# Kernel optimization log

Hardware: AMD Instinct MI355X
Metric: run time of the kernel (lower is better)

## Reference

```python
import jax, jax.numpy as jnp
import numpy as np
import math

PATCH = 16
IMG = 224
HEADS = 12
EMB = 768
HEAD_DIM = EMB // HEADS
SCALE = 1.0 / math.sqrt(HEAD_DIM)
NEG = -1.0e9


def _make_masks():
    n = IMG // PATCH  # patches per side
    centers = np.arange(n) * PATCH + PATCH / 2.0
    rows = np.repeat(centers, n)  # token center rows, length n*n
    cols = np.tile(centers, n)    # token center cols
    left = (cols[:, None] < cols[None, :]).astype(np.float32)
    right = (cols[:, None] > cols[None, :]).astype(np.float32)
    up = (rows[:, None] < rows[None, :]).astype(np.float32)
    down = (rows[:, None] > rows[None, :]).astype(np.float32)
    ident = np.eye(n * n, dtype=np.float32)
    pad = lambda m: np.pad(m, ((1, 0), (1, 0)))  # prepend CLS row/col of zeros
    return [jnp.asarray(pad(m)) for m in (left, right, up, down, ident)]

MASKS = _make_masks()  # 5 masks, each [N, N] with N = 197


def setup_inputs() -> dict:
    key = jax.random.key(0)
    ks = jax.random.split(key, 18)
    B, N = 32, (IMG // PATCH) ** 2 + 1
    w = lambda k: jax.random.normal(k, (EMB, EMB), jnp.float32) * 0.02
    b = lambda k: jax.random.normal(k, (EMB,), jnp.float32) * 0.02
    return {
        'x': jax.random.normal(ks[0], (B, N, EMB), jnp.float32),
        'q_w': w(ks[1]), 'q_b': b(ks[2]),
        'kA_w': w(ks[3]), 'kA_b': b(ks[4]),
        'kB_w': w(ks[5]), 'kB_b': b(ks[6]),
        'kC_w': w(ks[7]), 'kC_b': b(ks[8]),
        'kD_w': w(ks[9]), 'kD_b': b(ks[10]),
        'kE_w': w(ks[11]), 'kE_b': b(ks[12]),
        'v_w': w(ks[13]), 'v_b': b(ks[14]),
        'proj_w': w(ks[15]), 'proj_b': b(ks[16]),
    }


def reference(x, q_w, q_b, kA_w, kA_b, kB_w, kB_b, kC_w, kC_b, kD_w, kD_b,
              kE_w, kE_b, v_w, v_b, proj_w, proj_b):
    B, N, _ = x.shape
    # torch Linear: y = x @ W.T + b; then [B,N,H,D] -> [B,H,N,D]
    lin = lambda w, b_: (x @ w.T + b_).reshape(B, N, HEADS, HEAD_DIM).transpose(0, 2, 1, 3)
    q = lin(q_w, q_b) * SCALE
    v = lin(v_w, v_b)
    out = jnp.zeros_like(v)
    k_params = [(kA_w, kA_b), (kB_w, kB_b), (kC_w, kC_b), (kD_w, kD_b), (kE_w, kE_b)]
    for (kw, kb), mask in zip(k_params, MASKS):
        k = lin(kw, kb)
        scores = jnp.einsum('bhnd,bhmd->bhnm', q, k) + (1.0 - mask) * NEG
        out = out + jnp.einsum('bhnm,bhmd->bhnd', jax.nn.softmax(scores, axis=-1), v)
    out = out.transpose(0, 2, 1, 3).reshape(B, N, EMB)
    return out @ proj_w.T + proj_b
```

## Files before the change

### kernel.cpp

```cpp
#include <hip/hip_runtime.h>
#include <stdint.h>

typedef unsigned short u16;
typedef __bf16 bf16x8 __attribute__((ext_vector_type(8)));
typedef float f32x4 __attribute__((ext_vector_type(4)));

#define KDIM   768
#define MP     6400
#define MREAL  6304
#define SLOT   ((size_t)MP * KDIM)
#define WSZ    ((size_t)KDIM * KDIM)
#define QSCALE_L 0.18033688011112042f
#define BIGL     1.4426950e9f

struct Ptr9 { const float* p[9]; };
struct Ptr7 { const float* p[7]; };

__device__ __forceinline__ u16 f2b(float f) {
  uint32_t x = __float_as_uint(f);
  x += 0x7FFFu + ((x >> 16) & 1u);
  return (u16)(x >> 16);
}

__device__ __forceinline__ float b2f(u16 v) {
  return __uint_as_float(((uint32_t)v) << 16);
}

__device__ __forceinline__ void async16(const void* g, void* l) {
  __builtin_amdgcn_global_load_lds(
      (__attribute__((address_space(1))) void*)(uintptr_t)g,
      (__attribute__((address_space(3))) void*)l, 16, 0, 0);
}

__global__ __launch_bounds__(256) void k_convert(Ptr9 src, u16* __restrict__ xb,
                                                 u16* __restrict__ wall) {
  const int XN4 = MREAL * KDIM / 4;
  const int WN4 = (int)(WSZ / 4);
  const int total = XN4 + 8 * WN4;
  for (int i = blockIdx.x * blockDim.x + threadIdx.x; i < total;
       i += gridDim.x * blockDim.x) {
    const float4* sp; ushort4* dp; int off;
    if (i < XN4) { sp = (const float4*)src.p[0]; dp = (ushort4*)xb; off = i; }
    else {
      int t = i - XN4; int slot = t / WN4; off = t - slot * WN4;
      sp = (const float4*)src.p[1 + slot];
      dp = (ushort4*)(wall + (size_t)slot * WSZ);
    }
    float4 v = sp[off];
    ushort4 u;
    u.x = f2b(v.x); u.y = f2b(v.y); u.z = f2b(v.z); u.w = f2b(v.w);
    dp[off] = u;
  }
}

__global__ __launch_bounds__(256) void k_gemm(const u16* __restrict__ A,
                                              const u16* __restrict__ W,
                                              Ptr7 bias,
                                              u16* __restrict__ outb,
                                              float* __restrict__ outf,
                                              float scale0, int guard) {
  __shared__ u16 As[128 * 32];
  __shared__ u16 Bs[128 * 32];
  const int tid = threadIdx.x;
  const int w = tid >> 6, lane = tid & 63;
  const int li = lane & 15, g = lane >> 4;
  const int brow = blockIdx.x, bcol = blockIdx.y, z = blockIdx.z;
  const u16* Wz = W + (size_t)z * WSZ;
  const float* bz = bias.p[z];
  const int wr = (w >> 1) * 64, wc = (w & 1) * 64;
  f32x4 acc[4][4] = {};

  for (int k0 = 0; k0 < KDIM; k0 += 32) {
    __syncthreads();
#pragma unroll
    for (int c = 0; c < 2; ++c) {
      int cbase = (c * 4 + w) * 64;
      int chunk = cbase + lane;
      int row = chunk >> 2, kg = chunk & 3;
      async16(A  + (size_t)(brow * 128 + row) * KDIM + k0 + kg * 8,
              (char*)As + cbase * 16);
      async16(Wz + (size_t)(bcol * 128 + row) * KDIM + k0 + kg * 8,
              (char*)Bs + cbase * 16);
    }
    asm volatile("s_waitcnt vmcnt(0)" ::: "memory");
    __syncthreads();

    bf16x8 af[4], bfr[4];
#pragma unroll
    for (int i = 0; i < 4; ++i) {
      af[i]  = *(const bf16x8*)(As + (wr + i * 16 + li) * 32 + g * 8);
      bfr[i] = *(const bf16x8*)(Bs + (wc + i * 16 + li) * 32 + g * 8);
    }
#pragma unroll
    for (int i = 0; i < 4; ++i)
#pragma unroll
      for (int j = 0; j < 4; ++j)
        acc[i][j] = __builtin_amdgcn_mfma_f32_16x16x32_bf16(af[i], bfr[j],
                                                            acc[i][j], 0, 0, 0);
  }

  const float scz = (z == 0) ? scale0 : 1.0f;
  if (outf == nullptr) {
    u16* O = outb + (size_t)z * SLOT;
#pragma unroll
    for (int j = 0; j < 4; ++j) {
      int col = bcol * 128 + wc + j * 16 + li;
      float bsv = bz[col];
#pragma unroll
      for (int i = 0; i < 4; ++i) {
        int row = brow * 128 + wr + i * 16 + g * 4;
#pragma unroll
        for (int r = 0; r < 4; ++r)
          O[(size_t)(row + r) * KDIM + col] = f2b((acc[i][j][r] + bsv) * scz);
      }
    }
  } else {
#pragma unroll
    for (int j = 0; j < 4; ++j) {
      int col = bcol * 128 + wc + j * 16 + li;
      float bsv = bz[col];
#pragma unroll
      for (int i = 0; i < 4; ++i) {
        int row = brow * 128 + wr + i * 16 + g * 4;
#pragma unroll
        for (int r = 0; r < 4; ++r)
          if (row + r < guard)
            outf[(size_t)(row + r) * KDIM + col] = acc[i][j][r] + bsv;
      }
    }
  }
}

__global__ __launch_bounds__(512, 4) void k_attn(const u16* __restrict__ qkv,
                                                 u16* __restrict__ att) {
  __shared__ u16 KL[208 * 64];
  __shared__ u16 VT[64][228];
  __shared__ u16 P[2][8][16][36];
  const int tid = threadIdx.x;
  const int w = tid >> 6, lane = tid & 63;
  const int li = lane & 15, g = lane >> 4;
  const int bx = blockIdx.x, h = blockIdx.y, b = blockIdx.z;
  const int rt = bx * 8 + w;
  const size_t rowbase = (size_t)b * 197;
  const int cb = h * 64;
  const u16* Q = qkv;
  const u16* V = qkv + 6 * SLOT;
  const bool task = (rt <= 12);
  const int nmask = (bx == 0) ? 5 : 4;

  auto stageK = [&](int m) {
    const u16* Kg = qkv + (size_t)(1 + m) * SLOT;
#pragma unroll
    for (int i = 0; i < 4; ++i) {
      int cb64 = (i * 8 + w) * 64;
      if (cb64 >= 1664) break;
      int c = cb64 + lane;
      int row = c >> 3;
      int kg = (c & 7) ^ (row & 7);
      async16(Kg + (rowbase + row) * KDIM + cb + kg * 8,
              (char*)KL + cb64 * 16);
    }
  };

  stageK(0);

  for (int e = tid; e < 64 * 228; e += 512) {
    int j = e >> 6, d = e & 63;
    u16 val = 0;
    if (j < 197) val = V[(rowbase + j) * KDIM + cb + d];
    VT[d][j] = val;
  }

  const int i_ = rt * 16 + li;
  const int pi = i_ - 1;
  const int ri = pi / 14, ci = pi % 14;
  const bool i0 = (i_ == 0);

  const int rs_init = (g * 4 - 1) / 14;
  const int cs_init = (g * 4 - 1) % 14;

  bf16x8 qa0, qa1;
  {
    const size_t qrow = rowbase + (size_t)rt * 16 + li;
    qa0 = *(const bf16x8*)(Q + qrow * KDIM + cb + g * 8);
    qa1 = *(const bf16x8*)(Q + qrow * KDIM + cb + 32 + g * 8);
  }

  f32x4 oacc[4] = {};

  for (int m = 0; m < nmask; ++m) {
    asm volatile("s_waitcnt vmcnt(0)" ::: "memory");
    __syncthreads();

    const bool doit = task && (m < 4 || rt == 0);
    f32x4 s[13];
    if (doit) {
      __builtin_amdgcn_s_setprio(1);
#pragma unroll
      for (int t = 0; t < 13; ++t) {
        const char* base = (const char*)KL + (size_t)(t * 16 + li) * 128;
        const int sw = (li & 7) << 4;
        bf16x8 kb0 = *(const bf16x8*)(base + ((g * 16) ^ sw));
        bf16x8 kb1 = *(const bf16x8*)(base + ((64 + g * 16) ^ sw));
        f32x4 zz = {};
        zz = __builtin_amdgcn_mfma_f32_16x16x32_bf16(kb0, qa0, zz, 0, 0, 0);
        zz = __builtin_amdgcn_mfma_f32_16x16x32_bf16(kb1, qa1, zz, 0, 0, 0);
        s[t] = zz;
      }
      __builtin_amdgcn_s_setprio(0);
    }
    __syncthreads();
    if (m + 1 < nmask) stageK(m + 1);

    if (doit) {
      float mx = -3.0e38f;
      int cs = cs_init, rs = rs_init;
#pragma unroll
      for (int t = 0; t < 13; ++t) {
        int jv = t * 16 + g * 4;
        int cjr = cs, rjr = rs;
#pragma unroll
        for (int r = 0; r < 4; ++r) {
          bool mk;
          if (m == 0)      mk = ci < cjr;
          else if (m == 1) mk = ci > cjr;
          else if (m == 2) mk = ri < rjr;
          else if (m == 3) mk = ri > rjr;
          else             mk = (i_ == jv);
          if (i0 | (jv == 0)) mk = false;
          float sv = s[t][r] - (mk ? 0.f : BIGL);
          if (jv >= 197) sv = -3.0e38f;
          s[t][r] = sv;
          mx = fmaxf(mx, sv);
          ++jv; ++cjr; if (cjr == 14) { cjr = 0; ++rjr; }
        }
        cs += 2; ++rs; if (cs >= 14) { cs -= 14; ++rs; }
      }
      mx = fmaxf(mx, __shfl_xor(mx, 16));
      mx = fmaxf(mx, __shfl_xor(mx, 32));
      float sum = 0.f;
#pragma unroll
      for (int t = 0; t < 13; ++t)
#pragma unroll
        for (int r = 0; r < 4; ++r) {
          float e_ = exp2f(s[t][r] - mx);
          s[t][r] = e_;
          sum += e_;
        }
      sum += __shfl_xor(sum, 16);
      sum += __shfl_xor(sum, 32);
      const float inv = 1.0f / sum;

#pragma unroll
      for (int kt = 0; kt <= 7; ++kt) {
        if (kt < 7) {
#pragma unroll
          for (int h2 = 0; h2 < 2; ++h2) {
            const int t = kt * 2 + h2;
            uint32_t w0 = 0, w1 = 0;
            if (t < 13) {
              float a0 = s[t][0] * inv, a1 = s[t][1] * inv;
              float a2 = s[t][2] * inv, a3 = s[t][3] * inv;
              asm("v_cvt_pk_bf16_f32 %0, %1, %2" : "=v"(w0) : "v"(a0), "v"(a1));
              asm("v_cvt_pk_bf16_f32 %0, %1, %2" : "=v"(w1) : "v"(a2), "v"(a3));
            }
            uint2 pw; pw.x = w0; pw.y = w1;
            *(uint2*)&P[kt & 1][w][li][h2 * 16 + g * 4] = pw;
          }
        }
        if (kt > 0) {
          const int kr = kt - 1;
          bf16x8 pa = *(const bf16x8*)&P[kr & 1][w][li][g * 8];
          __builtin_amdgcn_s_setprio(1);
#pragma unroll
          for (int dt = 0; dt < 4; ++dt) {
            bf16x8 vb = *(const bf16x8*)&VT[dt * 16 + li][kr * 32 + g * 8];
            oacc[dt] = __builtin_amdgcn_mfma_f32_16x16x32_bf16(pa, vb, oacc[dt],
                                                               0, 0, 0);
          }
          __builtin_amdgcn_s_setprio(0);
        }
      }
    }
  }

  if (task && rt > 0) {
#pragma unroll
    for (int dt = 0; dt < 4; ++dt)
#pragma unroll
      for (int r = 0; r < 4; ++r) {
        int i2 = rt * 16 + g * 4 + r;
        oacc[dt][r] += b2f(VT[dt * 16 + li][i2]);
      }
  }

  if (task) {
#pragma unroll
    for (int dt = 0; dt < 4; ++dt)
#pragma unroll
      for (int r = 0; r < 4; ++r) {
        int i2 = rt * 16 + g * 4 + r;
        if (i2 < 197)
          att[(rowbase + i2) * KDIM + cb + dt * 16 + li] = f2b(oacc[dt][r]);
      }
  }
}

extern "C" void kernel_launch(void* const* d_in, const int* in_sizes, int n_in,
                              void* d_out, int out_size, void* d_ws, size_t ws_size,
                              hipStream_t stream) {
  (void)in_sizes; (void)n_in; (void)out_size; (void)ws_size;
  const float* x      = (const float*)d_in[0];
  const float* q_w    = (const float*)d_in[1];
  const float* q_b    = (const float*)d_in[2];
  const float* kA_w   = (const float*)d_in[3];
  const float* kA_b   = (const float*)d_in[4];
  const float* kB_w   = (const float*)d_in[5];
  const float* kB_b   = (const float*)d_in[6];
  const float* kC_w   = (const float*)d_in[7];
  const float* kC_b   = (const float*)d_in[8];
  const float* kD_w   = (const float*)d_in[9];
  const float* kD_b   = (const float*)d_in[10];
  const float* kE_w   = (const float*)d_in[11];
  const float* kE_b   = (const float*)d_in[12];
  const float* v_w    = (const float*)d_in[13];
  const float* v_b    = (const float*)d_in[14];
  const float* proj_w = (const float*)d_in[15];
  const float* proj_b = (const float*)d_in[16];
  float* out = (float*)d_out;

  u16* xb   = (u16*)d_ws;
  u16* qkv  = xb + SLOT;
  u16* wall = qkv + 7 * SLOT;
  u16* att  = xb;

  Ptr9 cs;
  cs.p[0] = x;    cs.p[1] = q_w;  cs.p[2] = kA_w; cs.p[3] = kB_w;
  cs.p[4] = kC_w; cs.p[5] = kD_w; cs.p[6] = kE_w; cs.p[7] = v_w;
  cs.p[8] = proj_w;
  k_convert<<<dim3(2048), dim3(256), 0, stream>>>(cs, xb, wall);

  Ptr7 b1;
  b1.p[0] = q_b;  b1.p[1] = kA_b; b1.p[2] = kB_b; b1.p[3] = kC_b;
  b1.p[4] = kD_b; b1.p[5] = kE_b; b1.p[6] = v_b;
  k_gemm<<<dim3(50, 6, 7), dim3(256), 0, stream>>>(xb, wall, b1, qkv, nullptr,
                                                   QSCALE_L, 0);

  k_attn<<<dim3(2, 12, 32), dim3(512), 0, stream>>>(qkv, att);

  Ptr7 b2;
  for (int i = 0; i < 7; ++i) b2.p[i] = proj_b;
  k_gemm<<<dim3(50, 6, 1), dim3(256), 0, stream>>>(att, wall + 7 * WSZ, b2,
                                                   nullptr, out, 1.0f, MREAL);
}
```

Baseline: 241.7 us.

## Keep softmax probabilities in registers by permuting V layout, drop P shared buffer

Removes the shared-memory round trip for the probability matrix. The softmax outputs are packed directly into MFMA A-operand registers, and V^T is stored in shared memory in a key-permuted, XOR-swizzled order that matches this register layout. It also vectorizes the V staging loads, shrinks the K and V shared buffers so the block needs less LDS, and raises the launch-bounds occupancy hint from 4 to 6. The permuted indexing adds address arithmetic and scattered 2-byte LDS stores during staging, and the higher occupancy target may constrain registers.

```diff
diff --git a/kernel.cpp b/kernel.cpp
--- a/kernel.cpp
+++ b/kernel.cpp
@@ -131,11 +131,11 @@
   }
 }
 
-__global__ __launch_bounds__(512, 4) void k_attn(const u16* __restrict__ qkv,
+__global__ __launch_bounds__(512, 6) void k_attn(const u16* __restrict__ qkv,
                                                  u16* __restrict__ att) {
-  __shared__ u16 KL[208 * 64];
-  __shared__ u16 VT[64][228];
-  __shared__ u16 P[2][8][16][36];
+  __shared__ u16 SM[200 * 64 + 64 * 224];
+  u16* KL = SM;
+  char* VTc = (char*)(SM + 200 * 64);
   const int tid = threadIdx.x;
   const int w = tid >> 6, lane = tid & 63;
   const int li = lane & 15, g = lane >> 4;
@@ -153,22 +153,34 @@
 #pragma unroll
     for (int i = 0; i < 4; ++i) {
       int cb64 = (i * 8 + w) * 64;
-      if (cb64 >= 1664) break;
-      int c = cb64 + lane;
-      int row = c >> 3;
-      int kg = (c & 7) ^ (row & 7);
-      async16(Kg + (rowbase + row) * KDIM + cb + kg * 8,
-              (char*)KL + cb64 * 16);
+      if (cb64 < 1600) {
+        int c = cb64 + lane;
+        int row = c >> 3;
+        int kg = (c & 7) ^ (row & 7);
+        async16(Kg + (rowbase + row) * KDIM + cb + kg * 8,
+                (char*)KL + cb64 * 16);
+      }
     }
   };
 
   stageK(0);
 
-  for (int e = tid; e < 64 * 228; e += 512) {
-    int j = e >> 6, d = e & 63;
-    u16 val = 0;
-    if (j < 197) val = V[(rowbase + j) * KDIM + cb + d];
-    VT[d][j] = val;
+  for (int e = tid; e < 224 * 8; e += 512) {
+    int j = e >> 3, d8 = e & 7;
+    uint4 vv = make_uint4(0, 0, 0, 0);
+    if (j < 197) vv = *(const uint4*)(V + (rowbase + j) * KDIM + cb + d8 * 8);
+    int t = j >> 4;
+    int k = (t >> 1) * 32 + ((j >> 2) & 3) * 8 + (t & 1) * 4 + (j & 3);
+    u16 hh[8];
+    hh[0] = (u16)vv.x; hh[1] = (u16)(vv.x >> 16);
+    hh[2] = (u16)vv.y; hh[3] = (u16)(vv.y >> 16);
+    hh[4] = (u16)vv.z; hh[5] = (u16)(vv.z >> 16);
+    hh[6] = (u16)vv.w; hh[7] = (u16)(vv.w >> 16);
+#pragma unroll
+    for (int q = 0; q < 8; ++q) {
+      int d = d8 * 8 + q;
+      *(u16*)(VTc + ((d * 448 + k * 2) ^ ((d & 3) << 4))) = hh[q];
+    }
   }
 
   const int i_ = rt * 16 + li;
@@ -251,35 +263,32 @@
       sum += __shfl_xor(sum, 32);
       const float inv = 1.0f / sum;
 
-#pragma unroll
-      for (int kt = 0; kt <= 7; ++kt) {
-        if (kt < 7) {
-#pragma unroll
-          for (int h2 = 0; h2 < 2; ++h2) {
-            const int t = kt * 2 + h2;
-            uint32_t w0 = 0, w1 = 0;
-            if (t < 13) {
-              float a0 = s[t][0] * inv, a1 = s[t][1] * inv;
-              float a2 = s[t][2] * inv, a3 = s[t][3] * inv;
-              asm("v_cvt_pk_bf16_f32 %0, %1, %2" : "=v"(w0) : "v"(a0), "v"(a1));
-              asm("v_cvt_pk_bf16_f32 %0, %1, %2" : "=v"(w1) : "v"(a2), "v"(a3));
-            }
-            uint2 pw; pw.x = w0; pw.y = w1;
-            *(uint2*)&P[kt & 1][w][li][h2 * 16 + g * 4] = pw;
-          }
+      union PU { uint32_t u[4]; bf16x8 v; };
+#pragma unroll
+      for (int kt = 0; kt < 7; ++kt) {
+        PU pu;
+        {
+          float a0 = s[2 * kt][0] * inv, a1 = s[2 * kt][1] * inv;
+          float a2 = s[2 * kt][2] * inv, a3 = s[2 * kt][3] * inv;
+          asm("v_cvt_pk_bf16_f32 %0, %1, %2" : "=v"(pu.u[0]) : "v"(a0), "v"(a1));
+          asm("v_cvt_pk_bf16_f32 %0, %1, %2" : "=v"(pu.u[1]) : "v"(a2), "v"(a3));
         }
-        if (kt > 0) {
-          const int kr = kt - 1;
-          bf16x8 pa = *(const bf16x8*)&P[kr & 1][w][li][g * 8];
-          __builtin_amdgcn_s_setprio(1);
-#pragma unroll
-          for (int dt = 0; dt < 4; ++dt) {
-            bf16x8 vb = *(const bf16x8*)&VT[dt * 16 + li][kr * 32 + g * 8];
-            oacc[dt] = __builtin_amdgcn_mfma_f32_16x16x32_bf16(pa, vb, oacc[dt],
-                                                               0, 0, 0);
-          }
-          __builtin_amdgcn_s_setprio(0);
+        if (kt < 6) {
+          float b0 = s[2 * kt + 1][0] * inv, b1 = s[2 * kt + 1][1] * inv;
+          float b2 = s[2 * kt + 1][2] * inv, b3 = s[2 * kt + 1][3] * inv;
+          asm("v_cvt_pk_bf16_f32 %0, %1, %2" : "=v"(pu.u[2]) : "v"(b0), "v"(b1));
+          asm("v_cvt_pk_bf16_f32 %0, %1, %2" : "=v"(pu.u[3]) : "v"(b2), "v"(b3));
+        } else { pu.u[2] = 0; pu.u[3] = 0; }
+        __builtin_amdgcn_s_setprio(1);
+#pragma unroll
+        for (int dt = 0; dt < 4; ++dt) {
+          int row = dt * 16 + li;
+          bf16x8 vb = *(const bf16x8*)(VTc +
+              ((row * 448 + kt * 64 + g * 16) ^ ((li & 3) << 4)));
+          oacc[dt] = __builtin_amdgcn_mfma_f32_16x16x32_bf16(pu.v, vb, oacc[dt],
+                                                             0, 0, 0);
         }
+        __builtin_amdgcn_s_setprio(0);
       }
     }
   }
@@ -290,7 +299,11 @@
 #pragma unroll
       for (int r = 0; r < 4; ++r) {
         int i2 = rt * 16 + g * 4 + r;
-        oacc[dt][r] += b2f(VT[dt * 16 + li][i2]);
+        int t2 = i2 >> 4;
+        int k2 = (t2 >> 1) * 32 + ((i2 >> 2) & 3) * 8 + (t2 & 1) * 4 + (i2 & 3);
+        int row = dt * 16 + li;
+        u16 hv = *(const u16*)(VTc + ((row * 448 + k2 * 2) ^ ((li & 3) << 4)));
+        oacc[dt][r] += b2f(hv);
       }
   }
 
```

Result: slower. 435.8 us (+80.3%).
